# Optimization experiments

Measured on AMD Instinct MI355X. Metric: run time of the kernel, lower is better.

## Reference

```python
import jax, jax.numpy as jnp
import numpy as np
import math

N_HEADS = 16
EMBD = 1024
D_HEAD = EMBD // N_HEADS


def setup_inputs() -> dict:
    key = jax.random.key(0)
    ks = jax.random.split(key, 5)
    s = 1.0 / math.sqrt(EMBD)
    return {
        "x": jax.random.normal(ks[0], (2, 2048, EMBD), dtype=jnp.float32),
        "w_in": jax.random.normal(ks[1], (EMBD, 3 * EMBD), dtype=jnp.float32) * s,
        "b_in": jax.random.normal(ks[2], (3 * EMBD,), dtype=jnp.float32) * 0.02,
        "w_out": jax.random.normal(ks[3], (EMBD, EMBD), dtype=jnp.float32) * s,
        "b_out": jax.random.normal(ks[4], (EMBD,), dtype=jnp.float32) * 0.02,
    }


def reference(x, w_in, b_in, w_out, b_out):
    # x: [B, S, D]
    B, S, D = x.shape
    qkv = x @ w_in + b_in                      # [B, S, 3D]
    q, k, v = jnp.split(qkv, 3, axis=-1)
    # [B, S, H, dh] -> [B, H, S, dh]
    def heads(t):
        return t.reshape(B, S, N_HEADS, D_HEAD).transpose(0, 2, 1, 3)
    q, k, v = heads(q), heads(k), heads(v)
    scores = jnp.einsum("bhqd,bhkd->bhqk", q, k)  # [B, H, S, S]
    # causal mask applied before scaling (as in original; -inf invariant to scale)
    causal = jnp.tril(jnp.ones((S, S), dtype=bool))
    scores = jnp.where(causal, scores, -jnp.inf)
    scores = scores / jnp.asarray(math.sqrt(D_HEAD), dtype=scores.dtype)
    attn = jax.nn.softmax(scores, axis=-1)
    out = jnp.einsum("bhqk,bhkd->bhqd", attn, v)  # [B, H, S, dh]
    out = out.transpose(0, 2, 1, 3).reshape(B, S, D)
    return out @ w_out + b_out
```

## Files before the change

### kernel.cpp

```cpp
#include <hip/hip_runtime.h>
#include <stdint.h>

#define DEVI __device__ __forceinline__

typedef __attribute__((ext_vector_type(8))) short short8;
typedef __attribute__((ext_vector_type(4))) float f32x4;

DEVI unsigned short f2bf(float f) {
    union { float f; uint32_t u; } v; v.f = f;
    return (unsigned short)((v.u + 0x7FFFu + ((v.u >> 16) & 1u)) >> 16);
}

DEVI uint32_t cvtpk_bf16(float a, float b) {
    uint32_t r;
    asm("v_cvt_pk_bf16_f32 %0, %1, %2" : "=v"(r) : "v"(a), "v"(b));
    return r;
}

DEVI void gload16(const void* g, void* l) {
    __builtin_amdgcn_global_load_lds(
        (const __attribute__((address_space(1))) unsigned int*)g,
        (__attribute__((address_space(3))) unsigned int*)l, 16, 0, 0);
}

__global__ void k_cvt(const float* __restrict__ in, ushort* __restrict__ out, int n4) {
    int i = blockIdx.x * blockDim.x + threadIdx.x;
    int stride = gridDim.x * blockDim.x;
    for (; i < n4; i += stride) {
        float4 v = ((const float4*)in)[i];
        ushort4 o;
        o.x = f2bf(v.x); o.y = f2bf(v.y); o.z = f2bf(v.z); o.w = f2bf(v.w);
        ((ushort4*)out)[i] = o;
    }
}

__global__ void k_tcvt(const float* __restrict__ in, ushort* __restrict__ out, int R, int C) {
    __shared__ float t[32][33];
    int c0 = blockIdx.x * 32, r0 = blockIdx.y * 32;
    int lr = threadIdx.x >> 5, lc = threadIdx.x & 31;
    #pragma unroll
    for (int i = 0; i < 4; i++)
        t[lr + 8*i][lc] = in[(size_t)(r0 + lr + 8*i)*C + c0 + lc];
    __syncthreads();
    #pragma unroll
    for (int i = 0; i < 4; i++)
        out[(size_t)(c0 + lr + 8*i)*R + r0 + lc] = f2bf(t[lc][lr + 8*i]);
}

template<int MODE>
__global__ __launch_bounds__(256, 2) void k_gemm(
    const ushort* __restrict__ A, const ushort* __restrict__ Bt,
    const float* __restrict__ bias,
    ushort* __restrict__ oQ, ushort* __restrict__ oK, ushort* __restrict__ oV,
    float* __restrict__ oF,
    int M, int N, int K, int S)
{
    __shared__ __align__(16) ushort As[128*64];
    __shared__ __align__(16) ushort Bs[128*64];
    const int tid = threadIdx.x;
    const int w = tid >> 6, l = tid & 63;
    const int m0 = blockIdx.y * 128, n0 = blockIdx.x * 128;
    const int wr = (w >> 1) * 64, wc = (w & 1) * 64;
    const int fr = l & 15, fg = l >> 4;
    const int lr8 = l >> 3;
    const int slot = (l & 7) ^ lr8;

    f32x4 acc[4][4] = {};

    const ushort* Abase = A + (size_t)(m0 + w*32 + lr8) * K + slot*8;
    const ushort* Bbase = Bt + (size_t)(n0 + w*32 + lr8) * K + slot*8;

    for (int k0 = 0; k0 < K; k0 += 64) {
        __syncthreads();
        #pragma unroll
        for (int i = 0; i < 4; i++) {
            gload16(Abase + (size_t)(8*i)*K + k0, &As[(w*32 + 8*i)*64]);
            gload16(Bbase + (size_t)(8*i)*K + k0, &Bs[(w*32 + 8*i)*64]);
        }
        __syncthreads();
        #pragma unroll
        for (int kk = 0; kk < 2; kk++) {
            short8 af[4], bfr[4];
            #pragma unroll
            for (int i = 0; i < 4; i++) {
                int ra = wr + i*16 + fr;
                af[i] = *(const short8*)((const char*)As + ra*128 + ((kk*64 + fg*16) ^ ((ra & 7) << 4)));
                int rb = wc + i*16 + fr;
                bfr[i] = *(const short8*)((const char*)Bs + rb*128 + ((kk*64 + fg*16) ^ ((rb & 7) << 4)));
            }
            #pragma unroll
            for (int i = 0; i < 4; i++)
                #pragma unroll
                for (int j = 0; j < 4; j++)
                    acc[i][j] = __builtin_amdgcn_mfma_f32_16x16x32_bf16(af[i], bfr[j], acc[i][j], 0, 0, 0);
        }
    }

    if (MODE == 1) {
        #pragma unroll
        for (int j = 0; j < 4; j++) {
            int n = n0 + wc + j*16 + fr;
            float bv = bias[n];
            #pragma unroll
            for (int i = 0; i < 4; i++) {
                int mrow = m0 + wr + i*16 + fg*4;
                #pragma unroll
                for (int r = 0; r < 4; r++)
                    oF[(size_t)(mrow + r)*N + n] = acc[i][j][r] + bv;
            }
        }
    } else {
        #pragma unroll
        for (int j = 0; j < 4; j++) {
            int n = n0 + wc + j*16 + fr;
            int region = n >> 10;
            int h = (n & 1023) >> 6;
            int d = n & 63;
            float bv = bias[n];
            float scl = (region == 0) ? 0.18033688011112042f : 1.0f;
            #pragma unroll
            for (int i = 0; i < 4; i++) {
                int mrow = m0 + wr + i*16 + fg*4;
                int b = mrow >> 11;
                int s = mrow & 2047;
                if (region < 2) {
                    ushort* dst = (region == 0 ? oQ : oK) + ((size_t)(b*16 + h)*S)*64 + (size_t)d;
                    #pragma unroll
                    for (int r = 0; r < 4; r++)
                        dst[(size_t)(s + r)*64] = f2bf((acc[i][j][r] + bv) * scl);
                } else {
                    ushort* dst = oV + ((size_t)(b*16 + h)*64 + d)*S + s;
                    ushort4 pk;
                    pk.x = f2bf(acc[i][j][0] + bv);
                    pk.y = f2bf(acc[i][j][1] + bv);
                    pk.z = f2bf(acc[i][j][2] + bv);
                    pk.w = f2bf(acc[i][j][3] + bv);
                    *(ushort4*)dst = pk;
                }
            }
        }
    }
}

__global__ __launch_bounds__(256, 2) void k_attn(
    const ushort* __restrict__ Q,
    const ushort* __restrict__ Kb,
    const ushort* __restrict__ Vt,
    ushort* __restrict__ O,
    int S)
{
    __shared__ __align__(16) ushort Kt[2][64*64];
    __shared__ __align__(16) ushort Vs[2][64*64];
    __shared__ __align__(16) ushort Ps[4][32*64];

    const int tid = threadIdx.x, w = tid >> 6, l = tid & 63;
    const int bid = blockIdx.x;
    const int half = bid >> 8;
    const int r_ = bid & 255;
    const int h = r_ & 15, b = (r_ >> 4) & 1, p = r_ >> 5;
    const int qi = half ? (15 - p) : p;
    const int bh = b * 16 + h;
    const int qw = qi * 128 + w * 32;
    const int fr = l & 15, fg = l >> 4;

    short8 qf[2][2];
    {
        const ushort* qp = Q + ((size_t)bh*S + qw + fr)*64 + fg*8;
        qf[0][0] = *(const short8*)(qp);
        qf[0][1] = *(const short8*)(qp + 32);
        qf[1][0] = *(const short8*)(qp + 16*64);
        qf[1][1] = *(const short8*)(qp + 16*64 + 32);
    }

    float l_[2] = {0.f, 0.f};
    f32x4 o_[2][4] = {};

    const int lr8 = l >> 3;
    const int slot = (l & 7) ^ lr8;
    const int rb0 = w * 16, rb1 = w * 16 + 8;
    const ushort* Ksrc = Kb + (size_t)bh*S*64;
    const ushort* Vsrc = Vt + (size_t)bh*64*S;

    const int nt = 2*qi + 2;

    auto stage = [&](int buf, int j0) {
        gload16(Ksrc + (size_t)(j0 + rb0 + lr8)*64 + slot*8, &Kt[buf][rb0*64]);
        gload16(Ksrc + (size_t)(j0 + rb1 + lr8)*64 + slot*8, &Kt[buf][rb1*64]);
        gload16(Vsrc + (size_t)(rb0 + lr8)*S + j0 + slot*8, &Vs[buf][rb0*64]);
        gload16(Vsrc + (size_t)(rb1 + lr8)*S + j0 + slot*8, &Vs[buf][rb1*64]);
    };

    stage(0, 0);
    __syncthreads();
    int cur = 0;

    for (int jt = 0; jt < nt; jt++) {
        const int j0 = jt * 64;
        if (jt + 1 < nt) stage(cur ^ 1, j0 + 64);

        f32x4 sa[2][4] = {};
        __builtin_amdgcn_s_setprio(1);
        #pragma unroll
        for (int kk = 0; kk < 2; kk++) {
            short8 kf[4];
            #pragma unroll
            for (int f = 0; f < 4; f++) {
                int row = f*16 + fr;
                kf[f] = *(const short8*)((const char*)Kt[cur] + row*128 + ((kk*64 + fg*16) ^ ((row & 7) << 4)));
            }
            #pragma unroll
            for (int t = 0; t < 2; t++)
                #pragma unroll
                for (int f = 0; f < 4; f++)
                    sa[t][f] = __builtin_amdgcn_mfma_f32_16x16x32_bf16(kf[f], qf[t][kk], sa[t][f], 0, 0, 0);
        }
        __builtin_amdgcn_s_setprio(0);

        if (jt >= 2*qi) {
            #pragma unroll
            for (int t = 0; t < 2; t++) {
                int qg = qw + t*16 + fr;
                #pragma unroll
                for (int f = 0; f < 4; f++) {
                    int base = j0 + f*16 + fg*4 - qg;
                    #pragma unroll
                    for (int r = 0; r < 4; r++)
                        if (base + r > 0) sa[t][f][r] = -1e30f;
                }
            }
        }

        #pragma unroll
        for (int t = 0; t < 2; t++) {
            char* pb = (char*)Ps[w] + (t*16 + fr)*128;
            const int sw = (fr & 3) << 5;
            #pragma unroll
            for (int f = 0; f < 4; f++) {
                float p0 = __builtin_amdgcn_exp2f(sa[t][f][0]);
                float p1 = __builtin_amdgcn_exp2f(sa[t][f][1]);
                float p2 = __builtin_amdgcn_exp2f(sa[t][f][2]);
                float p3 = __builtin_amdgcn_exp2f(sa[t][f][3]);
                l_[t] += (p0 + p1) + (p2 + p3);
                uint2 pk;
                pk.x = cvtpk_bf16(p0, p1);
                pk.y = cvtpk_bf16(p2, p3);
                *(uint2*)(pb + ((f*32 + fg*8) ^ sw)) = pk;
            }
        }

        __builtin_amdgcn_s_setprio(1);
        #pragma unroll
        for (int kk = 0; kk < 2; kk++) {
            short8 pf[2];
            #pragma unroll
            for (int t = 0; t < 2; t++) {
                int row = t*16 + fr;
                pf[t] = *(const short8*)((const char*)Ps[w] + row*128 + ((kk*64 + fg*16) ^ ((fr & 3) << 5)));
            }
            #pragma unroll
            for (int f = 0; f < 4; f++) {
                int row = f*16 + fr;
                short8 vf = *(const short8*)((const char*)Vs[cur] + row*128 + ((kk*64 + fg*16) ^ ((row & 7) << 4)));
                #pragma unroll
                for (int t = 0; t < 2; t++)
                    o_[t][f] = __builtin_amdgcn_mfma_f32_16x16x32_bf16(vf, pf[t], o_[t][f], 0, 0, 0);
            }
        }
        __builtin_amdgcn_s_setprio(0);

        __syncthreads();
        cur ^= 1;
    }

    #pragma unroll
    for (int t = 0; t < 2; t++) {
        l_[t] += __shfl_xor(l_[t], 16);
        l_[t] += __shfl_xor(l_[t], 32);
    }

    #pragma unroll
    for (int t = 0; t < 2; t++) {
        float inv = 1.0f / l_[t];
        int qg = qw + t*16 + fr;
        #pragma unroll
        for (int f = 0; f < 4; f++) {
            ushort4 pk;
            pk.x = f2bf(o_[t][f][0] * inv);
            pk.y = f2bf(o_[t][f][1] * inv);
            pk.z = f2bf(o_[t][f][2] * inv);
            pk.w = f2bf(o_[t][f][3] * inv);
            *(ushort4*)&O[((size_t)(b*S + qg))*1024 + h*64 + f*16 + fg*4] = pk;
        }
    }
}

extern "C" void kernel_launch(void* const* d_in, const int* in_sizes, int n_in,
                              void* d_out, int out_size, void* d_ws, size_t ws_size,
                              hipStream_t stream)
{
    const float* x     = (const float*)d_in[0];
    const float* w_in  = (const float*)d_in[1];
    const float* b_in  = (const float*)d_in[2];
    const float* w_out = (const float*)d_in[3];
    const float* b_out = (const float*)d_in[4];
    float* out = (float*)d_out;

    const int B = 2, S = 2048, D = 1024, H = 16;
    const int M = B * S;

    if (ws_size < (40u << 20)) return;
    char* ws = (char*)d_ws;
    ushort* xb     = (ushort*)(ws);
    ushort* w_inT  = (ushort*)(ws + (8u << 20));
    ushort* w_outT = (ushort*)(ws + (14u << 20));
    ushort* qb     = (ushort*)(ws + (16u << 20));
    ushort* kb     = (ushort*)(ws + (24u << 20));
    ushort* vtb    = (ushort*)(ws + (32u << 20));

    k_cvt<<<2048, 256, 0, stream>>>(x, xb, M*D/4);
    k_tcvt<<<dim3(3*D/32, D/32), 256, 0, stream>>>(w_in, w_inT, D, 3*D);
    k_tcvt<<<dim3(D/32, D/32), 256, 0, stream>>>(w_out, w_outT, D, D);
    k_gemm<0><<<dim3(3*D/128, M/128), 256, 0, stream>>>(xb, w_inT, b_in, qb, kb, vtb, nullptr, M, 3*D, D, S);
    k_attn<<<512, 256, 0, stream>>>(qb, kb, vtb, xb, S);
    k_gemm<1><<<dim3(D/128, M/128), 256, 0, stream>>>(xb, w_outT, b_out, nullptr, nullptr, nullptr, out, M, D, D, S);
}
```

Before: 113.6 us.

## Shrink attention blocks to 64 rows, use permlane for P, swizzle GEMM tiles

The attention kernel now runs 1024 blocks of 128 threads, each covering 64 query rows. That roughly halves the wasted masked tiles on the diagonal and gives finer causal load balancing, with the longest tiles scheduled first. The P matrix no longer round-trips through LDS: v_permlane32/16_swap instructions rearrange the packed bf16 probabilities in registers into the MFMA operand layout, which drops the Ps scratch buffer. The GEMM kernels also get a blockwise tile swizzle meant to improve L2 locality. In exchange, each attention block stages K and V with fewer threads and does more issue work per wave.

```diff
diff --git a/kernel.cpp b/kernel.cpp
--- a/kernel.cpp
+++ b/kernel.cpp
@@ -5,6 +5,7 @@
 
 typedef __attribute__((ext_vector_type(8))) short short8;
 typedef __attribute__((ext_vector_type(4))) float f32x4;
+typedef __attribute__((ext_vector_type(4))) uint32_t u32x4;
 
 DEVI unsigned short f2bf(float f) {
     union { float f; uint32_t u; } v; v.f = f;
@@ -15,6 +16,13 @@
     uint32_t r;
     asm("v_cvt_pk_bf16_f32 %0, %1, %2" : "=v"(r) : "v"(a), "v"(b));
     return r;
+}
+
+DEVI void perm32(uint32_t &a, uint32_t &b) {
+    asm("v_permlane32_swap_b32 %0, %1" : "+v"(a), "+v"(b));
+}
+DEVI void perm16(uint32_t &a, uint32_t &b) {
+    asm("v_permlane16_swap_b32 %0, %1" : "+v"(a), "+v"(b));
 }
 
 DEVI void gload16(const void* g, void* l) {
@@ -59,7 +67,12 @@
     __shared__ __align__(16) ushort Bs[128*64];
     const int tid = threadIdx.x;
     const int w = tid >> 6, l = tid & 63;
-    const int m0 = blockIdx.y * 128, n0 = blockIdx.x * 128;
+
+    int lin = blockIdx.y * gridDim.x + blockIdx.x;
+    int nwg = gridDim.x * gridDim.y;
+    int swz = (lin & 7) * (nwg >> 3) + (lin >> 3);
+    const int m0 = (swz / gridDim.x) * 128, n0 = (swz % gridDim.x) * 128;
+
     const int wr = (w >> 1) * 64, wc = (w & 1) * 64;
     const int fr = l & 15, fg = l >> 4;
     const int lr8 = l >> 3;
@@ -142,7 +155,7 @@
     }
 }
 
-__global__ __launch_bounds__(256, 2) void k_attn(
+__global__ __launch_bounds__(128, 2) void k_attn(
     const ushort* __restrict__ Q,
     const ushort* __restrict__ Kb,
     const ushort* __restrict__ Vt,
@@ -151,16 +164,15 @@
 {
     __shared__ __align__(16) ushort Kt[2][64*64];
     __shared__ __align__(16) ushort Vs[2][64*64];
-    __shared__ __align__(16) ushort Ps[4][32*64];
 
     const int tid = threadIdx.x, w = tid >> 6, l = tid & 63;
     const int bid = blockIdx.x;
-    const int half = bid >> 8;
-    const int r_ = bid & 255;
+    const int half = bid >> 9;
+    const int r_ = bid & 511;
     const int h = r_ & 15, b = (r_ >> 4) & 1, p = r_ >> 5;
-    const int qi = half ? (15 - p) : p;
+    const int qt = half ? p : (31 - p);
     const int bh = b * 16 + h;
-    const int qw = qi * 128 + w * 32;
+    const int qw = qt * 64 + w * 32;
     const int fr = l & 15, fg = l >> 4;
 
     short8 qf[2][2];
@@ -177,17 +189,18 @@
 
     const int lr8 = l >> 3;
     const int slot = (l & 7) ^ lr8;
-    const int rb0 = w * 16, rb1 = w * 16 + 8;
     const ushort* Ksrc = Kb + (size_t)bh*S*64;
     const ushort* Vsrc = Vt + (size_t)bh*64*S;
 
-    const int nt = 2*qi + 2;
+    const int nt = qt + 1;
 
     auto stage = [&](int buf, int j0) {
-        gload16(Ksrc + (size_t)(j0 + rb0 + lr8)*64 + slot*8, &Kt[buf][rb0*64]);
-        gload16(Ksrc + (size_t)(j0 + rb1 + lr8)*64 + slot*8, &Kt[buf][rb1*64]);
-        gload16(Vsrc + (size_t)(rb0 + lr8)*S + j0 + slot*8, &Vs[buf][rb0*64]);
-        gload16(Vsrc + (size_t)(rb1 + lr8)*S + j0 + slot*8, &Vs[buf][rb1*64]);
+        #pragma unroll
+        for (int i = 0; i < 4; i++) {
+            int rb = w*32 + i*8;
+            gload16(Ksrc + (size_t)(j0 + rb + lr8)*64 + slot*8, &Kt[buf][rb*64]);
+            gload16(Vsrc + (size_t)(rb + lr8)*S + j0 + slot*8, &Vs[buf][rb*64]);
+        }
     };
 
     stage(0, 0);
@@ -216,7 +229,7 @@
         }
         __builtin_amdgcn_s_setprio(0);
 
-        if (jt >= 2*qi) {
+        if (jt == nt - 1) {
             #pragma unroll
             for (int t = 0; t < 2; t++) {
                 int qg = qw + t*16 + fr;
@@ -230,10 +243,9 @@
             }
         }
 
-        #pragma unroll
-        for (int t = 0; t < 2; t++) {
-            char* pb = (char*)Ps[w] + (t*16 + fr)*128;
-            const int sw = (fr & 3) << 5;
+        uint32_t cw[2][4][2];
+        #pragma unroll
+        for (int t = 0; t < 2; t++)
             #pragma unroll
             for (int f = 0; f < 4; f++) {
                 float p0 = __builtin_amdgcn_exp2f(sa[t][f][0]);
@@ -241,12 +253,9 @@
                 float p2 = __builtin_amdgcn_exp2f(sa[t][f][2]);
                 float p3 = __builtin_amdgcn_exp2f(sa[t][f][3]);
                 l_[t] += (p0 + p1) + (p2 + p3);
-                uint2 pk;
-                pk.x = cvtpk_bf16(p0, p1);
-                pk.y = cvtpk_bf16(p2, p3);
-                *(uint2*)(pb + ((f*32 + fg*8) ^ sw)) = pk;
-            }
-        }
+                cw[t][f][0] = cvtpk_bf16(p0, p1);
+                cw[t][f][1] = cvtpk_bf16(p2, p3);
+            }
 
         __builtin_amdgcn_s_setprio(1);
         #pragma unroll
@@ -254,8 +263,12 @@
             short8 pf[2];
             #pragma unroll
             for (int t = 0; t < 2; t++) {
-                int row = t*16 + fr;
-                pf[t] = *(const short8*)((const char*)Ps[w] + row*128 + ((kk*64 + fg*16) ^ ((fr & 3) << 5)));
+                uint32_t a0 = cw[t][2*kk][0], b0 = cw[t][2*kk + 1][0];
+                perm32(a0, b0); perm16(a0, b0);
+                uint32_t a1 = cw[t][2*kk][1], b1 = cw[t][2*kk + 1][1];
+                perm32(a1, b1); perm16(a1, b1);
+                u32x4 uw; uw[0] = a0; uw[1] = a1; uw[2] = b0; uw[3] = b1;
+                pf[t] = __builtin_bit_cast(short8, uw);
             }
             #pragma unroll
             for (int f = 0; f < 4; f++) {
@@ -321,6 +334,6 @@
     k_tcvt<<<dim3(3*D/32, D/32), 256, 0, stream>>>(w_in, w_inT, D, 3*D);
     k_tcvt<<<dim3(D/32, D/32), 256, 0, stream>>>(w_out, w_outT, D, D);
     k_gemm<0><<<dim3(3*D/128, M/128), 256, 0, stream>>>(xb, w_inT, b_in, qb, kb, vtb, nullptr, M, 3*D, D, S);
-    k_attn<<<512, 256, 0, stream>>>(qb, kb, vtb, xb, S);
+    k_attn<<<1024, 128, 0, stream>>>(qb, kb, vtb, xb, S);
     k_gemm<1><<<dim3(D/128, M/128), 256, 0, stream>>>(xb, w_outT, b_out, nullptr, nullptr, nullptr, out, M, D, D, S);
 }
```

After: 110.9 us. 2.4% less time.
